# Kernel tuning notes

Measured on AMD Instinct MI355X. Metric: run time of the kernel, lower is better.

## Reference

```python
import jax, jax.numpy as jnp
import numpy as np

N_NODES, N_EDGES, F_IN = 8192, 32768, 16
N_SUB, N_GRAPH = 512, 32
EDGE_DIM, HID = 5, 128
DIMS = [(16, 32), (32, 64), (64, 64)]  # (M_in, M_out) per NNConv layer


def _segment_mean(x, seg, n):
    s = jax.ops.segment_sum(x, seg, num_segments=n)
    c = jax.ops.segment_sum(jnp.ones((x.shape[0], 1), x.dtype), seg, num_segments=n)
    return s / jnp.maximum(c, 1.0)


def _nnconv(x, src, dst, eattr, W1, b1, W2, b2, root, bias):
    # edge MLP -> per-edge weight matrix theta: [E, M_in, M_out]
    h = jax.nn.relu(eattr @ W1 + b1)
    theta = (h @ W2 + b2).reshape(-1, x.shape[1], root.shape[1])
    msg = jnp.einsum('ei,eio->eo', x[src], theta)          # gather + per-edge matvec
    agg = jax.ops.segment_sum(msg, dst, num_segments=x.shape[0])  # scatter-add (aggr='add')
    return agg + x @ root + bias


def setup_inputs() -> dict:
    key = jax.random.key(0)
    ks = jax.random.split(key, 32)
    inp = {}
    inp['x'] = jax.random.normal(ks[0], (N_NODES, F_IN), jnp.float32)
    inp['edge_index'] = jax.random.randint(ks[1], (2, N_EDGES), 0, N_NODES)
    inp['edge_attr'] = jax.random.uniform(ks[2], (N_EDGES, EDGE_DIM), jnp.float32)
    inp['node_to_subgraph'] = jnp.sort(jax.random.randint(ks[3], (N_NODES,), 0, N_SUB))
    inp['subgraph_to_graph'] = jnp.sort(jax.random.randint(ks[4], (N_SUB,), 0, N_GRAPH))
    i = 5
    for l, (ci, co) in enumerate(DIMS):
        inp[f'W1_{l}'] = jax.random.normal(ks[i], (EDGE_DIM, HID), jnp.float32) * 0.1
        inp[f'b1_{l}'] = jnp.zeros((HID,), jnp.float32)
        inp[f'W2_{l}'] = jax.random.normal(ks[i + 1], (HID, ci * co), jnp.float32) * 0.05
        inp[f'b2_{l}'] = jnp.zeros((ci * co,), jnp.float32)
        inp[f'root_{l}'] = jax.random.normal(ks[i + 2], (ci, co), jnp.float32) * 0.1
        inp[f'bias_{l}'] = jnp.zeros((co,), jnp.float32)
        i += 3
    inp['fc1_w'] = jax.random.normal(ks[i], (64, 32), jnp.float32) * 0.1
    inp['fc1_b'] = jnp.zeros((32,), jnp.float32)
    inp['fc2_w'] = jax.random.normal(ks[i + 1], (32, 16), jnp.float32) * 0.1
    inp['fc2_b'] = jnp.zeros((16,), jnp.float32)
    inp['fc3_w'] = jax.random.normal(ks[i + 2], (16, 1), jnp.float32) * 0.1
    inp['fc3_b'] = jnp.zeros((1,), jnp.float32)
    return inp


def reference(x, edge_index, edge_attr, node_to_subgraph, subgraph_to_graph,
              W1_0, b1_0, W2_0, b2_0, root_0, bias_0,
              W1_1, b1_1, W2_1, b2_1, root_1, bias_1,
              W1_2, b1_2, W2_2, b2_2, root_2, bias_2,
              fc1_w, fc1_b, fc2_w, fc2_b, fc3_w, fc3_b):
    src, dst = edge_index[0], edge_index[1]
    layers = [(W1_0, b1_0, W2_0, b2_0, root_0, bias_0),
              (W1_1, b1_1, W2_1, b2_1, root_1, bias_1),
              (W1_2, b1_2, W2_2, b2_2, root_2, bias_2)]
    h = x
    for (W1, b1, W2, b2, root, bias) in layers:
        h = jax.nn.elu(_nnconv(h, src, dst, edge_attr, W1, b1, W2, b2, root, bias))
    h = _segment_mean(h, node_to_subgraph, N_SUB)      # global_mean_pool over subgraphs
    h = _segment_mean(h, subgraph_to_graph, N_GRAPH)   # global_mean_pool over graphs
    h = jax.nn.elu(h @ fc1_w + fc1_b)
    h = jax.nn.elu(h @ fc2_w + fc2_b)
    return (h @ fc3_w + fc3_b).reshape(-1)
```

## Files before the change

### kernel.cpp

```cpp
#include <hip/hip_runtime.h>

#define E_EDGES 32768
#define NN 8192
#define HID 128
#define KS 2

typedef _Float16 half8 __attribute__((ext_vector_type(8)));
typedef float f32x4 __attribute__((ext_vector_type(4)));

__global__ void zero_init_k(int* __restrict__ hist, float* __restrict__ pools, int npool) {
  int t = blockIdx.x * 256 + threadIdx.x;
  if (t < NN) hist[t] = 0;
  if (t < npool) pools[t] = 0.f;
}

__global__ void hist_k(const int* __restrict__ dst, int* __restrict__ hist) {
  int e = blockIdx.x * 256 + threadIdx.x;
  if (e < E_EDGES) atomicAdd(&hist[dst[e]], 1);
}

__global__ void scan_k(const int* __restrict__ hist, int* __restrict__ roff, int* __restrict__ cursor) {
  __shared__ int ps[1024];
  int t = threadIdx.x;
  int loc[8]; int s = 0;
  int base = t * 8;
#pragma unroll
  for (int j = 0; j < 8; ++j) { loc[j] = s; s += hist[base + j]; }
  ps[t] = s;
  __syncthreads();
  for (int off = 1; off < 1024; off <<= 1) {
    int v = 0;
    if (t >= off) v = ps[t - off];
    __syncthreads();
    if (t >= off) ps[t] += v;
    __syncthreads();
  }
  int excl = (t == 0) ? 0 : ps[t - 1];
#pragma unroll
  for (int j = 0; j < 8; ++j) { int v = excl + loc[j]; roff[base + j] = v; cursor[base + j] = v; }
  if (t == 1023) roff[NN] = ps[1023];
}

__global__ void scatter_k(const int* __restrict__ dst, int* __restrict__ cursor, int* __restrict__ eidx) {
  int e = blockIdx.x * 256 + threadIdx.x;
  if (e < E_EDGES) { int p = atomicAdd(&cursor[dst[e]], 1); eidx[p] = e; }
}

template <int CI, int CO>
__global__ void prep_b_k(const float* __restrict__ W2, const float* __restrict__ b2,
                         _Float16* __restrict__ out) {
  constexpr int Kmain = 128 * CI;
  constexpr int Kpad = (Kmain + CI + 31) & ~31;
  int idx = blockIdx.x * 256 + threadIdx.x;
  if (idx >= Kpad * CO) return;
  int j = idx & 7;
  int n = (idx >> 3) & (CO - 1);
  int kg = idx >> (3 + (CO == 64 ? 6 : 5));
  int k = kg * 8 + j;
  float v = 0.f;
  if (k < Kmain) {
    int h = k / CI, i = k & (CI - 1);
    v = W2[(h * CI + i) * CO + n];
  } else if (k < Kmain + CI) {
    int tt = k - Kmain;
    v = b2[tt * CO + n];
  }
  out[idx] = (_Float16)v;
}

template <int CI, int CO>
__launch_bounds__(256, 2)
__global__ void msg_mfma_k(const float* __restrict__ xcur, const int* __restrict__ src,
                           const float* __restrict__ eattr, const float* __restrict__ W1,
                           const float* __restrict__ b1, const _Float16* __restrict__ Bsw,
                           float* __restrict__ msgbuf) {
  constexpr int ME = 128;
  constexpr int L2CI = (CI == 64) ? 6 : ((CI == 32) ? 5 : 4);
  constexpr int Kmain = 128 * CI;
  constexpr int Kpad = (Kmain + CI + 31) & ~31;
  constexpr int NK = Kpad / 32;
  constexpr int CSPLIT = 2 * CI;
  constexpr int XSTR = CI + 8;
  constexpr int SBH = 32 * CO;
  constexpr int FC = CO / 16;
  constexpr int NV4 = SBH / 8;

  __shared__ _Float16 he_s[64 * ME];
  __shared__ _Float16 xs_s[ME * XSTR];
  __shared__ _Float16 w2_s[2 * SBH];
  __shared__ float ea_s[ME * 5];
  __shared__ float W1s[5 * 64];
  __shared__ float b1s[64];
  __shared__ int src_s[ME];

  int t = threadIdx.x;
  int e0 = blockIdx.x * ME;
  int y = blockIdx.y;
  int hbeg = y * 64;

  for (int j = t; j < ME * 5; j += 256) ea_s[j] = eattr[e0 * 5 + j];
  for (int j = t; j < 5 * 64; j += 256) W1s[j] = W1[(j >> 6) * HID + hbeg + (j & 63)];
  if (t < 64) b1s[t] = b1[hbeg + t];
  if (t < ME) src_s[t] = src[e0 + t];
  __syncthreads();

  for (int j = t; j < 64 * ME; j += 256) {
    int hl = j >> 7, e = j & 127;
    float v = b1s[hl];
#pragma unroll
    for (int d = 0; d < 5; ++d) v += ea_s[e * 5 + d] * W1s[d * 64 + hl];
    he_s[hl * ME + e] = (_Float16)fmaxf(v, 0.f);
  }
  for (int j = t; j < ME * CI; j += 256) {
    int e = j >> L2CI, i = j & (CI - 1);
    xs_s[e * XSTR + i] = (_Float16)xcur[src_s[e] * CI + i];
  }
  int cbeg = y ? CSPLIT : 0;
  int cend = y ? NK : CSPLIT;
  if (t < NV4) ((float4*)w2_s)[t] = ((const float4*)(Bsw + (size_t)cbeg * SBH))[t];
  __syncthreads();

  int lane = t & 63;
  int w = t >> 6;
  int quad = lane >> 4, l15 = lane & 15;
  int eA0 = w * 32 + l15;

  f32x4 acc[2][FC];
#pragma unroll
  for (int fr = 0; fr < 2; ++fr)
#pragma unroll
    for (int fc = 0; fc < FC; ++fc)
#pragma unroll
      for (int r = 0; r < 4; ++r) acc[fr][fc][r] = 0.f;

  for (int c = cbeg; c < cend; ++c) {
    int p = (c - cbeg) & 1;
    float4 pf;
    bool more = (c + 1 < cend);
    if (more && t < NV4) pf = ((const float4*)(Bsw + (size_t)(c + 1) * SBH))[t];

    int kq = c * 32 + quad * 8;
    int i = kq & (CI - 1);
    half8 a[2];
    if (c * 32 < Kmain) {
      int hr = (kq >> L2CI) - hbeg;
#pragma unroll
      for (int fr = 0; fr < 2; ++fr) {
        int e = eA0 + 16 * fr;
        _Float16 hv = he_s[hr * ME + e];
        half8 xv = *(const half8*)&xs_s[e * XSTR + i];
        a[fr] = xv * hv;
      }
    } else {
#pragma unroll
      for (int fr = 0; fr < 2; ++fr) {
        int e = eA0 + 16 * fr;
        a[fr] = *(const half8*)&xs_s[e * XSTR + i];
      }
    }
    const _Float16* wb = w2_s + p * SBH + quad * (CO * 8);
#pragma unroll
    for (int fc = 0; fc < FC; ++fc) {
      half8 b = *(const half8*)&wb[(fc * 16 + l15) * 8];
      acc[0][fc] = __builtin_amdgcn_mfma_f32_16x16x32_f16(a[0], b, acc[0][fc], 0, 0, 0);
      acc[1][fc] = __builtin_amdgcn_mfma_f32_16x16x32_f16(a[1], b, acc[1][fc], 0, 0, 0);
    }
    __syncthreads();
    if (more && t < NV4) ((float4*)(w2_s + (1 - p) * SBH))[t] = pf;
    __syncthreads();
  }

  float* mb = msgbuf + ((size_t)y * E_EDGES + e0) * CO;
#pragma unroll
  for (int fr = 0; fr < 2; ++fr)
#pragma unroll
    for (int fc = 0; fc < FC; ++fc)
#pragma unroll
      for (int r = 0; r < 4; ++r) {
        int el = w * 32 + fr * 16 + quad * 4 + r;
        int o = fc * 16 + l15;
        mb[el * CO + o] = acc[fr][fc][r];
      }
}

template <int CI, int CO>
__global__ void gather_elu_k(const float* __restrict__ xcur, const float* __restrict__ root,
                             const float* __restrict__ bias, const float* __restrict__ msgbuf,
                             const int* __restrict__ roff, const int* __restrict__ eidx,
                             float* __restrict__ xnext) {
  constexpr int NB = 256 / CO;
  __shared__ float xs[NB * CI];
  int t = threadIdx.x;
  int n0 = blockIdx.x * NB;
  for (int j = t; j < NB * CI; j += 256) xs[j] = xcur[n0 * CI + j];
  __syncthreads();
  int nl = t / CO, o = t & (CO - 1);
  int n = n0 + nl;
  float a = bias[o];
#pragma unroll
  for (int i = 0; i < CI; ++i) a += xs[nl * CI + i] * root[i * CO + o];
  int j1 = roff[n + 1];
  for (int j = roff[n]; j < j1; ++j) {
    int e = eidx[j];
    a += msgbuf[(size_t)e * CO + o] + msgbuf[((size_t)E_EDGES + e) * CO + o];
  }
  xnext[n * CO + o] = a > 0.f ? a : expm1f(a);
}

__global__ void pool_sub_k(const float* __restrict__ x3, const int* __restrict__ n2s,
                           float* __restrict__ ssum, float* __restrict__ scnt) {
  int idx = blockIdx.x * 256 + threadIdx.x;
  int n = idx >> 6, o = idx & 63;
  int s = n2s[n];
  atomicAdd(&ssum[(s << 6) + o], x3[idx]);
  if (o == 0) atomicAdd(&scnt[s], 1.f);
}

__global__ void pool_graph_k(const float* __restrict__ ssum, const float* __restrict__ scnt,
                             const int* __restrict__ s2g, float* __restrict__ gsum,
                             float* __restrict__ gcnt) {
  int idx = blockIdx.x * 256 + threadIdx.x;
  int s = idx >> 6, o = idx & 63;
  int g = s2g[s];
  float v = ssum[idx] / fmaxf(scnt[s], 1.f);
  atomicAdd(&gsum[(g << 6) + o], v);
  if (o == 0) atomicAdd(&gcnt[g], 1.f);
}

__global__ void head_k(const float* __restrict__ gsum, const float* __restrict__ gcnt,
                       const float* __restrict__ w1, const float* __restrict__ b1,
                       const float* __restrict__ w2, const float* __restrict__ b2,
                       const float* __restrict__ w3, const float* __restrict__ b3,
                       float* __restrict__ out) {
  int g = blockIdx.x;
  int t = threadIdx.x;
  __shared__ float m[64], s1[32], s2[16];
  float c = fmaxf(gcnt[g], 1.f);
  m[t] = gsum[g * 64 + t] / c;
  __syncthreads();
  if (t < 32) {
    float a = b1[t];
    for (int i = 0; i < 64; ++i) a += m[i] * w1[i * 32 + t];
    s1[t] = a > 0.f ? a : expm1f(a);
  }
  __syncthreads();
  if (t < 16) {
    float a = b2[t];
    for (int i = 0; i < 32; ++i) a += s1[i] * w2[i * 16 + t];
    s2[t] = a > 0.f ? a : expm1f(a);
  }
  __syncthreads();
  if (t == 0) {
    float a = b3[0];
    for (int i = 0; i < 16; ++i) a += s2[i] * w3[i];
    out[g] = a;
  }
}

extern "C" void kernel_launch(void* const* d_in, const int* in_sizes, int n_in,
                              void* d_out, int out_size, void* d_ws, size_t ws_size,
                              hipStream_t stream) {
  (void)in_sizes; (void)n_in; (void)out_size; (void)ws_size;
  const float* x0 = (const float*)d_in[0];
  const int* ei = (const int*)d_in[1];
  const float* ea = (const float*)d_in[2];
  const int* n2s = (const int*)d_in[3];
  const int* s2g = (const int*)d_in[4];
  const float* W1_[3] = {(const float*)d_in[5], (const float*)d_in[11], (const float*)d_in[17]};
  const float* b1_[3] = {(const float*)d_in[6], (const float*)d_in[12], (const float*)d_in[18]};
  const float* W2_[3] = {(const float*)d_in[7], (const float*)d_in[13], (const float*)d_in[19]};
  const float* b2_[3] = {(const float*)d_in[8], (const float*)d_in[14], (const float*)d_in[20]};
  const float* rt_[3] = {(const float*)d_in[9], (const float*)d_in[15], (const float*)d_in[21]};
  const float* bs_[3] = {(const float*)d_in[10], (const float*)d_in[16], (const float*)d_in[22]};
  const float* fc1w = (const float*)d_in[23]; const float* fc1b = (const float*)d_in[24];
  const float* fc2w = (const float*)d_in[25]; const float* fc2b = (const float*)d_in[26];
  const float* fc3w = (const float*)d_in[27]; const float* fc3b = (const float*)d_in[28];
  float* out = (float*)d_out;

  const int* srcp = ei;
  const int* dstp = ei + E_EDGES;

  char* wsb = (char*)d_ws;
  size_t off = 0;
  auto alloc = [&](size_t bytes) {
    void* p = wsb + off;
    off += (bytes + 255) & ~(size_t)255;
    return p;
  };
  _Float16* Bsw0 = (_Float16*)alloc((size_t)2080 * 32 * 2);
  _Float16* Bsw1 = (_Float16*)alloc((size_t)4128 * 64 * 2);
  _Float16* Bsw2 = (_Float16*)alloc((size_t)8256 * 64 * 2);
  float* msgbuf = (float*)alloc((size_t)KS * E_EDGES * 64 * 4);
  float* x1 = (float*)alloc((size_t)NN * 32 * 4);
  float* x2 = (float*)alloc((size_t)NN * 64 * 4);
  float* x3 = (float*)alloc((size_t)NN * 64 * 4);
  int* hist = (int*)alloc((size_t)NN * 4);
  int* roff = (int*)alloc((size_t)(NN + 1) * 4);
  int* cursor = (int*)alloc((size_t)NN * 4);
  int* eidx = (int*)alloc((size_t)E_EDGES * 4);
  const int npool = 512 * 64 + 512 + 32 * 64 + 32;
  float* pools = (float*)alloc((size_t)npool * 4);
  float* ssum = pools;
  float* scnt = pools + 512 * 64;
  float* gsum = scnt + 512;
  float* gcnt = gsum + 32 * 64;

  zero_init_k<<<(npool + 255) / 256, 256, 0, stream>>>(hist, pools, npool);
  hist_k<<<E_EDGES / 256, 256, 0, stream>>>(dstp, hist);
  scan_k<<<1, 1024, 0, stream>>>(hist, roff, cursor);
  scatter_k<<<E_EDGES / 256, 256, 0, stream>>>(dstp, cursor, eidx);
  prep_b_k<16, 32><<<(2080 * 32 + 255) / 256, 256, 0, stream>>>(W2_[0], b2_[0], Bsw0);
  prep_b_k<32, 64><<<(4128 * 64 + 255) / 256, 256, 0, stream>>>(W2_[1], b2_[1], Bsw1);
  prep_b_k<64, 64><<<(8256 * 64 + 255) / 256, 256, 0, stream>>>(W2_[2], b2_[2], Bsw2);

  dim3 mg(E_EDGES / 128, KS);
  msg_mfma_k<16, 32><<<mg, 256, 0, stream>>>(x0, srcp, ea, W1_[0], b1_[0], Bsw0, msgbuf);
  gather_elu_k<16, 32><<<NN / 8, 256, 0, stream>>>(x0, rt_[0], bs_[0], msgbuf, roff, eidx, x1);
  msg_mfma_k<32, 64><<<mg, 256, 0, stream>>>(x1, srcp, ea, W1_[1], b1_[1], Bsw1, msgbuf);
  gather_elu_k<32, 64><<<NN / 4, 256, 0, stream>>>(x1, rt_[1], bs_[1], msgbuf, roff, eidx, x2);
  msg_mfma_k<64, 64><<<mg, 256, 0, stream>>>(x2, srcp, ea, W1_[2], b1_[2], Bsw2, msgbuf);
  gather_elu_k<64, 64><<<NN / 4, 256, 0, stream>>>(x2, rt_[2], bs_[2], msgbuf, roff, eidx, x3);

  pool_sub_k<<<NN * 64 / 256, 256, 0, stream>>>(x3, n2s, ssum, scnt);
  pool_graph_k<<<512 * 64 / 256, 256, 0, stream>>>(ssum, scnt, s2g, gsum, gcnt);
  head_k<<<32, 64, 0, stream>>>(gsum, gcnt, fc1w, fc1b, fc2w, fc2b, fc3w, fc3b, out);
}
```

Before: 296.0 us.

## Stream B fragments from global into registers, double edge tile, four-way K split

```diff
diff --git a/kernel.cpp b/kernel.cpp
--- a/kernel.cpp
+++ b/kernel.cpp
@@ -3,9 +3,10 @@
 #define E_EDGES 32768
 #define NN 8192
 #define HID 128
-#define KS 2
+#define KS 4
 
 typedef _Float16 half8 __attribute__((ext_vector_type(8)));
+typedef _Float16 half4 __attribute__((ext_vector_type(4)));
 typedef float f32x4 __attribute__((ext_vector_type(4)));
 
 __global__ void zero_init_k(int* __restrict__ hist, float* __restrict__ pools, int npool) {
@@ -50,7 +51,9 @@
 __global__ void prep_b_k(const float* __restrict__ W2, const float* __restrict__ b2,
                          _Float16* __restrict__ out) {
   constexpr int Kmain = 128 * CI;
-  constexpr int Kpad = (Kmain + CI + 31) & ~31;
+  constexpr int SPLITK = 32 * CI;
+  constexpr int TAILK = ((SPLITK + CI + 127) / 128) * 128;
+  constexpr int Kpad = 3 * SPLITK + TAILK;
   int idx = blockIdx.x * 256 + threadIdx.x;
   if (idx >= Kpad * CO) return;
   int j = idx & 7;
@@ -74,110 +77,113 @@
                            const float* __restrict__ eattr, const float* __restrict__ W1,
                            const float* __restrict__ b1, const _Float16* __restrict__ Bsw,
                            float* __restrict__ msgbuf) {
-  constexpr int ME = 128;
+  constexpr int ME = 256;
   constexpr int L2CI = (CI == 64) ? 6 : ((CI == 32) ? 5 : 4);
   constexpr int Kmain = 128 * CI;
-  constexpr int Kpad = (Kmain + CI + 31) & ~31;
-  constexpr int NK = Kpad / 32;
-  constexpr int CSPLIT = 2 * CI;
+  constexpr int SPLITK = 32 * CI;
+  constexpr int TAILK = ((SPLITK + CI + 127) / 128) * 128;
   constexpr int XSTR = CI + 8;
-  constexpr int SBH = 32 * CO;
   constexpr int FC = CO / 16;
-  constexpr int NV4 = SBH / 8;
-
-  __shared__ _Float16 he_s[64 * ME];
+  constexpr int C4 = CI / 4;
+  constexpr int L2C4 = L2CI - 2;
+
+  __shared__ _Float16 he_s[32 * ME];
   __shared__ _Float16 xs_s[ME * XSTR];
-  __shared__ _Float16 w2_s[2 * SBH];
   __shared__ float ea_s[ME * 5];
-  __shared__ float W1s[5 * 64];
-  __shared__ float b1s[64];
+  __shared__ float W1s[5 * 32];
+  __shared__ float b1s[32];
   __shared__ int src_s[ME];
 
   int t = threadIdx.x;
   int e0 = blockIdx.x * ME;
   int y = blockIdx.y;
-  int hbeg = y * 64;
+  int hbeg = y * 32;
 
   for (int j = t; j < ME * 5; j += 256) ea_s[j] = eattr[e0 * 5 + j];
-  for (int j = t; j < 5 * 64; j += 256) W1s[j] = W1[(j >> 6) * HID + hbeg + (j & 63)];
-  if (t < 64) b1s[t] = b1[hbeg + t];
-  if (t < ME) src_s[t] = src[e0 + t];
-  __syncthreads();
-
-  for (int j = t; j < 64 * ME; j += 256) {
-    int hl = j >> 7, e = j & 127;
+  if (t < 5 * 32) W1s[t] = W1[(t >> 5) * HID + hbeg + (t & 31)];
+  if (t < 32) b1s[t] = b1[hbeg + t];
+  src_s[t] = src[e0 + t];
+  __syncthreads();
+
+  for (int j = t; j < 32 * ME; j += 256) {
+    int hl = j / ME, e = j & (ME - 1);
     float v = b1s[hl];
 #pragma unroll
-    for (int d = 0; d < 5; ++d) v += ea_s[e * 5 + d] * W1s[d * 64 + hl];
+    for (int d = 0; d < 5; ++d) v += ea_s[e * 5 + d] * W1s[d * 32 + hl];
     he_s[hl * ME + e] = (_Float16)fmaxf(v, 0.f);
   }
-  for (int j = t; j < ME * CI; j += 256) {
-    int e = j >> L2CI, i = j & (CI - 1);
-    xs_s[e * XSTR + i] = (_Float16)xcur[src_s[e] * CI + i];
-  }
-  int cbeg = y ? CSPLIT : 0;
-  int cend = y ? NK : CSPLIT;
-  if (t < NV4) ((float4*)w2_s)[t] = ((const float4*)(Bsw + (size_t)cbeg * SBH))[t];
+  for (int j = t; j < ME * C4; j += 256) {
+    int e = j >> L2C4, i4 = j & (C4 - 1);
+    float4 v = ((const float4*)xcur)[src_s[e] * C4 + i4];
+    half4 hq = {(_Float16)v.x, (_Float16)v.y, (_Float16)v.z, (_Float16)v.w};
+    *(half4*)&xs_s[e * XSTR + i4 * 4] = hq;
+  }
   __syncthreads();
 
   int lane = t & 63;
   int w = t >> 6;
   int quad = lane >> 4, l15 = lane & 15;
-  int eA0 = w * 32 + l15;
-
-  f32x4 acc[2][FC];
-#pragma unroll
-  for (int fr = 0; fr < 2; ++fr)
+
+  int cbeg = y * (SPLITK / 32);
+  int cend = cbeg + ((y < 3) ? (SPLITK / 32) : (TAILK / 32));
+  int nrounds = (cend - cbeg) >> 2;
+
+  const half8* bsw8 = (const half8*)Bsw;
+  int ib = quad * CO + l15;
+
+  f32x4 acc[4][FC];
+#pragma unroll
+  for (int fr = 0; fr < 4; ++fr)
 #pragma unroll
     for (int fc = 0; fc < FC; ++fc)
 #pragma unroll
       for (int r = 0; r < 4; ++r) acc[fr][fc][r] = 0.f;
 
-  for (int c = cbeg; c < cend; ++c) {
-    int p = (c - cbeg) & 1;
-    float4 pf;
-    bool more = (c + 1 < cend);
-    if (more && t < NV4) pf = ((const float4*)(Bsw + (size_t)(c + 1) * SBH))[t];
-
-    int kq = c * 32 + quad * 8;
-    int i = kq & (CI - 1);
-    half8 a[2];
-    if (c * 32 < Kmain) {
+  half8 breg[4][FC];
+#pragma unroll
+  for (int j = 0; j < 4; ++j)
+#pragma unroll
+    for (int fc = 0; fc < FC; ++fc)
+      breg[j][fc] = bsw8[(cbeg + j) * 4 * CO + ib + fc * 16];
+
+  for (int r = 0; r < nrounds; ++r) {
+#pragma unroll
+    for (int j = 0; j < 4; ++j) {
+      int c = cbeg + r * 4 + j;
+      int kq = c * 32 + quad * 8;
+      int i = kq & (CI - 1);
       int hr = (kq >> L2CI) - hbeg;
-#pragma unroll
-      for (int fr = 0; fr < 2; ++fr) {
-        int e = eA0 + 16 * fr;
-        _Float16 hv = he_s[hr * ME + e];
+      half8 a[4];
+#pragma unroll
+      for (int fr = 0; fr < 4; ++fr) {
+        int e = w * 64 + fr * 16 + l15;
         half8 xv = *(const half8*)&xs_s[e * XSTR + i];
+        _Float16 hv = (_Float16)1.f;
+        if (kq < Kmain) hv = he_s[hr * ME + e];
         a[fr] = xv * hv;
       }
-    } else {
-#pragma unroll
-      for (int fr = 0; fr < 2; ++fr) {
-        int e = eA0 + 16 * fr;
-        a[fr] = *(const half8*)&xs_s[e * XSTR + i];
+#pragma unroll
+      for (int fc = 0; fc < FC; ++fc) {
+#pragma unroll
+        for (int fr = 0; fr < 4; ++fr)
+          acc[fr][fc] = __builtin_amdgcn_mfma_f32_16x16x32_f16(a[fr], breg[j][fc], acc[fr][fc], 0, 0, 0);
       }
+      int cn = c + 4;
+      if (cn >= cend) cn = cend - 1;
+#pragma unroll
+      for (int fc = 0; fc < FC; ++fc)
+        breg[j][fc] = bsw8[cn * 4 * CO + ib + fc * 16];
     }
-    const _Float16* wb = w2_s + p * SBH + quad * (CO * 8);
-#pragma unroll
-    for (int fc = 0; fc < FC; ++fc) {
-      half8 b = *(const half8*)&wb[(fc * 16 + l15) * 8];
-      acc[0][fc] = __builtin_amdgcn_mfma_f32_16x16x32_f16(a[0], b, acc[0][fc], 0, 0, 0);
-      acc[1][fc] = __builtin_amdgcn_mfma_f32_16x16x32_f16(a[1], b, acc[1][fc], 0, 0, 0);
-    }
-    __syncthreads();
-    if (more && t < NV4) ((float4*)(w2_s + (1 - p) * SBH))[t] = pf;
-    __syncthreads();
   }
 
   float* mb = msgbuf + ((size_t)y * E_EDGES + e0) * CO;
 #pragma unroll
-  for (int fr = 0; fr < 2; ++fr)
+  for (int fr = 0; fr < 4; ++fr)
 #pragma unroll
     for (int fc = 0; fc < FC; ++fc)
 #pragma unroll
       for (int r = 0; r < 4; ++r) {
-        int el = w * 32 + fr * 16 + quad * 4 + r;
+        int el = w * 64 + fr * 16 + quad * 4 + r;
         int o = fc * 16 + l15;
         mb[el * CO + o] = acc[fr][fc][r];
       }
@@ -202,7 +208,10 @@
   int j1 = roff[n + 1];
   for (int j = roff[n]; j < j1; ++j) {
     int e = eidx[j];
-    a += msgbuf[(size_t)e * CO + o] + msgbuf[((size_t)E_EDGES + e) * CO + o];
+    float m = 0.f;
+#pragma unroll
+    for (int s = 0; s < KS; ++s) m += msgbuf[((size_t)s * E_EDGES + e) * CO + o];
+    a += m;
   }
   xnext[n * CO + o] = a > 0.f ? a : expm1f(a);
 }
@@ -287,9 +296,9 @@
     off += (bytes + 255) & ~(size_t)255;
     return p;
   };
-  _Float16* Bsw0 = (_Float16*)alloc((size_t)2080 * 32 * 2);
-  _Float16* Bsw1 = (_Float16*)alloc((size_t)4128 * 64 * 2);
-  _Float16* Bsw2 = (_Float16*)alloc((size_t)8256 * 64 * 2);
+  _Float16* Bsw0 = (_Float16*)alloc((size_t)2176 * 32 * 2);
+  _Float16* Bsw1 = (_Float16*)alloc((size_t)4224 * 64 * 2);
+  _Float16* Bsw2 = (_Float16*)alloc((size_t)8320 * 64 * 2);
   float* msgbuf = (float*)alloc((size_t)KS * E_EDGES * 64 * 4);
   float* x1 = (float*)alloc((size_t)NN * 32 * 4);
   float* x2 = (float*)alloc((size_t)NN * 64 * 4);
@@ -309,11 +318,11 @@
   hist_k<<<E_EDGES / 256, 256, 0, stream>>>(dstp, hist);
   scan_k<<<1, 1024, 0, stream>>>(hist, roff, cursor);
   scatter_k<<<E_EDGES / 256, 256, 0, stream>>>(dstp, cursor, eidx);
-  prep_b_k<16, 32><<<(2080 * 32 + 255) / 256, 256, 0, stream>>>(W2_[0], b2_[0], Bsw0);
-  prep_b_k<32, 64><<<(4128 * 64 + 255) / 256, 256, 0, stream>>>(W2_[1], b2_[1], Bsw1);
-  prep_b_k<64, 64><<<(8256 * 64 + 255) / 256, 256, 0, stream>>>(W2_[2], b2_[2], Bsw2);
-
-  dim3 mg(E_EDGES / 128, KS);
+  prep_b_k<16, 32><<<(2176 * 32 + 255) / 256, 256, 0, stream>>>(W2_[0], b2_[0], Bsw0);
+  prep_b_k<32, 64><<<(4224 * 64 + 255) / 256, 256, 0, stream>>>(W2_[1], b2_[1], Bsw1);
+  prep_b_k<64, 64><<<(8320 * 64 + 255) / 256, 256, 0, stream>>>(W2_[2], b2_[2], Bsw2);
+
+  dim3 mg(E_EDGES / 256, KS);
   msg_mfma_k<16, 32><<<mg, 256, 0, stream>>>(x0, srcp, ea, W1_[0], b1_[0], Bsw0, msgbuf);
   gather_elu_k<16, 32><<<NN / 8, 256, 0, stream>>>(x0, rt_[0], bs_[0], msgbuf, roff, eidx, x1);
   msg_mfma_k<32, 64><<<mg, 256, 0, stream>>>(x1, srcp, ea, W1_[1], b1_[1], Bsw1, msgbuf);
```

New measurement: 269.6 us. 1.1x faster.
